# Performance work log

Hardware: AMD Instinct MI355X
Metric: run time of the kernel (lower is better)

The kernel has to match this reference:

```python
import jax, jax.numpy as jnp
import numpy as np

D_MSA = 256
D_PAIR = 128
N_HEADS = 8
HEAD_DIM = D_MSA // N_HEADS
EPS = 1e-5


def setup_inputs() -> dict:
    key = jax.random.key(0)
    ks = jax.random.split(key, 14)
    s = 0.02
    return {
        "msa": jax.random.normal(ks[0], (1, 64, 256, D_MSA), dtype=jnp.float32),
        "pair": jax.random.normal(ks[1], (1, 256, 256, D_PAIR), dtype=jnp.float32),
        "Wq": jax.random.normal(ks[2], (D_MSA, D_MSA), dtype=jnp.float32) * s,
        "bq": jnp.zeros((D_MSA,), jnp.float32),
        "Wk": jax.random.normal(ks[3], (D_MSA, D_MSA), dtype=jnp.float32) * s,
        "bk": jnp.zeros((D_MSA,), jnp.float32),
        "Wv": jax.random.normal(ks[4], (D_MSA, D_MSA), dtype=jnp.float32) * s,
        "bv": jnp.zeros((D_MSA,), jnp.float32),
        "Wpb": jax.random.normal(ks[5], (D_PAIR, N_HEADS), dtype=jnp.float32) * s,
        "bpb": jnp.zeros((N_HEADS,), jnp.float32),
        "Wo": jax.random.normal(ks[6], (D_MSA, D_MSA), dtype=jnp.float32) * s,
        "bo": jnp.zeros((D_MSA,), jnp.float32),
        "gamma": jnp.ones((D_MSA,), jnp.float32),
        "beta": jnp.zeros((D_MSA,), jnp.float32),
    }


def reference(msa, pair, Wq, bq, Wk, bk, Wv, bv, Wpb, bpb, Wo, bo, gamma, beta):
    B, N, L, D = msa.shape
    H, Hd = N_HEADS, HEAD_DIM
    # projections -> (B, N, L, H, Hd)
    q = (msa @ Wq + bq).reshape(B, N, L, H, Hd)
    k = (msa @ Wk + bk).reshape(B, N, L, H, Hd)
    v = (msa @ Wv + bv).reshape(B, N, L, H, Hd)
    # scores: (B, N, H, L, L)
    scores = jnp.einsum('bnihd,bnjhd->bnhij', q, k) / jnp.sqrt(jnp.float32(Hd))
    # pair bias: (B, L, L, H) -> (B, H, L, L), broadcast over N
    pb = jnp.transpose(pair @ Wpb + bpb, (0, 3, 1, 2))
    scores = scores + pb[:, None]
    attn = jax.nn.softmax(scores, axis=-1)
    attn_out = jnp.einsum('bnhij,bnjhd->bnihd', attn, v).reshape(B, N, L, D)
    attn_out = attn_out @ Wo + bo
    # residual + LayerNorm
    x = msa + attn_out
    mu = jnp.mean(x, axis=-1, keepdims=True)
    var = jnp.var(x, axis=-1, keepdims=True)
    return (x - mu) * jax.lax.rsqrt(var + EPS) * gamma + beta
```

## Files before the change

### kernel.cpp

```cpp
#include <hip/hip_runtime.h>

#define NSEQ 64
#define LL   256
#define DD   256
#define HH   8
#define HDIM 32

typedef short short8  __attribute__((ext_vector_type(8)));
typedef short short4v __attribute__((ext_vector_type(4)));
typedef float float4v __attribute__((ext_vector_type(4)));

#define MFMA16(a,b,c) __builtin_amdgcn_mfma_f32_16x16x32_bf16((a),(b),(c),0,0,0)

__device__ __forceinline__ float4v zero4() {
  float4v z;
  z[0] = 0.f; z[1] = 0.f; z[2] = 0.f; z[3] = 0.f;
  return z;
}

__device__ __forceinline__ short f2b(float f) {
  unsigned u = __float_as_uint(f);
  u = (u + 0x7fffu + ((u >> 16) & 1u)) >> 16;
  return (short)u;
}

__device__ __forceinline__ float b2f(short s) {
  return __uint_as_float(((unsigned)(unsigned short)s) << 16);
}

__device__ __forceinline__ short8 cvt8(const float* p) {
  float4 a = *(const float4*)p;
  float4 b = *(const float4*)(p + 4);
  short8 r;
  r[0] = f2b(a.x); r[1] = f2b(a.y); r[2] = f2b(a.z); r[3] = f2b(a.w);
  r[4] = f2b(b.x); r[5] = f2b(b.y); r[6] = f2b(b.z); r[7] = f2b(b.w);
  return r;
}

__device__ __forceinline__ void ld_lds16(const void* g, void* l) {
  __builtin_amdgcn_global_load_lds(
      (const __attribute__((address_space(1))) unsigned int*)g,
      (__attribute__((address_space(3))) unsigned int*)l, 16, 0, 0);
}
#define WAIT_VM0() __builtin_amdgcn_s_waitcnt(0x0F70)

#define WT_OFF    0
#define PB_OFF    (4*65536*2)
#define PBF_OFF   (PB_OFF + 8*65536*2)
#define Q_OFF     (PB_OFF + 8*65536*4)
#define K_OFF     (Q_OFF  + 16384*256*2)
#define VT_OFF    (K_OFF  + 16384*256*2)
#define MSA16_OFF (VT_OFF + 16384*256*2)
#define O_OFF     MSA16_OFF

__global__ __launch_bounds__(256) void k1_prep(
    const float* __restrict__ msa,  const float* __restrict__ pair,
    const float* __restrict__ Wq,   const float* __restrict__ Wk,
    const float* __restrict__ Wv,   const float* __restrict__ Wpb,
    const float* __restrict__ bpb,  const float* __restrict__ Wo,
    char* __restrict__ ws)
{
  __shared__ short ldsWt[16 * 136];
  int bx = blockIdx.x, tid = threadIdx.x;
  if (bx < 256) {
    short* pb16 = (short*)(ws + PB_OFF);
    for (int i = tid; i < 16 * 136; i += 256) ldsWt[i] = 0;
    __syncthreads();
    {
      float4 wv4 = *(const float4*)&Wpb[tid * 4];
      int kk = (tid * 4) >> 3, n0 = (tid * 4) & 7;
      ldsWt[(n0 + 0) * 136 + kk] = f2b(wv4.x);
      ldsWt[(n0 + 1) * 136 + kk] = f2b(wv4.y);
      ldsWt[(n0 + 2) * 136 + kk] = f2b(wv4.z);
      ldsWt[(n0 + 3) * 136 + kk] = f2b(wv4.w);
    }
    __syncthreads();
    int w = tid >> 6, l = tid & 63, q = l >> 4, c = l & 15;
    int base = bx * 256 + w * 64;
    float bias = bpb[c & 7];
    short8 bf[4];
#pragma unroll
    for (int ks = 0; ks < 4; ks++)
      bf[ks] = *(const short8*)&ldsWt[c * 136 + ks * 32 + q * 8];
    float4v acc[4];
#pragma unroll
    for (int mt = 0; mt < 4; mt++) acc[mt] = zero4();
#pragma unroll
    for (int ks = 0; ks < 4; ks++) {
#pragma unroll
      for (int mt = 0; mt < 4; mt++) {
        short8 af = cvt8(&pair[(base + mt * 16 + c) * 128 + ks * 32 + q * 8]);
        acc[mt] = MFMA16(af, bf[ks], acc[mt]);
      }
    }
    if (c < 8) {
#pragma unroll
      for (int mt = 0; mt < 4; mt++) {
        short4v o;
#pragma unroll
        for (int r = 0; r < 4; r++) o[r] = f2b(acc[mt][r] + bias);
        *(short4v*)&pb16[c * 65536 + base + mt * 16 + q * 4] = o;
      }
    }
  } else if (bx < 1280) {
    int b2 = bx - 256;
    int mat = b2 >> 8, r = b2 & 255;
    const float* W = (mat == 0) ? Wq : (mat == 1) ? Wk : (mat == 2) ? Wv : Wo;
    short* wt = (short*)(ws + WT_OFF) + mat * 65536;
    wt[tid * 256 + r] = f2b(W[r * 256 + tid]);
  } else {
    int b3 = bx - 1280;
    const float* src = msa + b3 * 8192;
    short* dst = (short*)(ws + MSA16_OFF) + b3 * 8192;
#pragma unroll
    for (int i = 0; i < 8; i++) {
      int idx = i * 1024 + tid * 4;
      float4 v = *(const float4*)&src[idx];
      short4v s;
      s[0] = f2b(v.x); s[1] = f2b(v.y); s[2] = f2b(v.z); s[3] = f2b(v.w);
      *(short4v*)&dst[idx] = s;
    }
  }
}

__global__ __launch_bounds__(256) void k2_qkv(
    const float* __restrict__ bq, const float* __restrict__ bk,
    const float* __restrict__ bv, char* __restrict__ ws)
{
  __shared__ __align__(16) short lsA[128 * 128];
  __shared__ __align__(16) short lsB[128 * 128];
  int bx = blockIdx.x, tid = threadIdx.x;
  if (bx >= 768) {
    int b = bx - 768;
    int it16 = b & 15;
    const short* src = (const short*)(ws + PB_OFF) + (b >> 4) * 65536 + it16 * 4096;
    short* pbf = (short*)(ws + PBF_OFF);
    short* lt = lsA;
#pragma unroll
    for (int i2 = 0; i2 < 2; i2++) {
      int idx = i2 * 2048 + tid * 8;
      *(short8*)&lt[(idx >> 8) * 264 + (idx & 255)] = *(const short8*)&src[idx];
    }
    __syncthreads();
#pragma unroll
    for (int i2 = 0; i2 < 4; i2++) {
      int fid = i2 * 256 + tid;
      int jt = fid >> 6, lane = fid & 63;
      int qp = lane >> 4, cp = lane & 15;
      short4v v;
#pragma unroll
      for (int r = 0; r < 4; r++)
        v[r] = lt[(qp * 4 + r) * 264 + jt * 16 + cp];
      *(short4v*)&pbf[((b * 16 + jt) * 64 + lane) * 4] = v;
    }
    return;
  }
  int rt = bx & 127, ct = bx >> 7;
  int m = ct >> 1, cb = (ct & 1) * 128;
  int R0 = rt * 128;
  const short* msa16 = (const short*)(ws + MSA16_OFF);
  const short* wt = (const short*)(ws + WT_OFF) + m * 65536;
  int w = tid >> 6, l = tid & 63, q = l >> 4, c = l & 15;
  int WR = (w & 1) * 64, WC = (w >> 1) * 64;
  float4v acc[4][4];
#pragma unroll
  for (int mt = 0; mt < 4; mt++)
#pragma unroll
    for (int nt = 0; nt < 4; nt++) acc[mt][nt] = zero4();

#pragma unroll 1
  for (int kk = 0; kk < 2; kk++) {
    if (kk) __syncthreads();
#pragma unroll
    for (int i = 0; i < 8; i++) {
      int ci = i * 256 + tid;
      int r = ci >> 4, pos = ci & 15;
      int kc = pos ^ (r & 7);
      ld_lds16(&msa16[(R0 + r) * 256 + kk * 128 + kc * 8], &lsA[ci * 8]);
    }
#pragma unroll
    for (int i = 0; i < 8; i++) {
      int ci = i * 256 + tid;
      int r = ci >> 4, pos = ci & 15;
      int kc = pos ^ (r & 7);
      ld_lds16(&wt[(cb + r) * 256 + kk * 128 + kc * 8], &lsB[ci * 8]);
    }
    WAIT_VM0();
    __syncthreads();
#pragma unroll
    for (int ks = 0; ks < 4; ks++) {
      short8 af[4], bf[4];
#pragma unroll
      for (int mt = 0; mt < 4; mt++) {
        int r = WR + mt * 16 + c;
        int phys = (ks * 4 + q) ^ (r & 7);
        af[mt] = *(const short8*)&lsA[r * 128 + phys * 8];
      }
#pragma unroll
      for (int nt = 0; nt < 4; nt++) {
        int r = WC + nt * 16 + c;
        int phys = (ks * 4 + q) ^ (r & 7);
        bf[nt] = *(const short8*)&lsB[r * 128 + phys * 8];
      }
#pragma unroll
      for (int mt = 0; mt < 4; mt++)
#pragma unroll
        for (int nt = 0; nt < 4; nt++)
          acc[mt][nt] = MFMA16(af[mt], bf[nt], acc[mt][nt]);
    }
  }

  const float* bp = (m == 0) ? bq : (m == 1) ? bk : bv;
  int n = R0 >> 8;
  if (m < 2) {
    short* dst = (short*)(ws + (m == 0 ? Q_OFF : K_OFF));
#pragma unroll
    for (int nt = 0; nt < 4; nt++) {
      int ch = cb + WC + nt * 16 + c;
      float bb = bp[ch];
      int h = ch >> 5, hd = ch & 31;
#pragma unroll
      for (int mt = 0; mt < 4; mt++) {
        int i0 = (R0 & 255) + WR + mt * 16 + q * 4;
#pragma unroll
        for (int r = 0; r < 4; r++)
          dst[((n * HH + h) * 256 + i0 + r) * HDIM + hd] = f2b(acc[mt][nt][r] + bb);
      }
    }
  } else {
    short* vt = (short*)(ws + VT_OFF);
#pragma unroll
    for (int nt = 0; nt < 4; nt++) {
      int ch = cb + WC + nt * 16 + c;
      float bb = bp[ch];
#pragma unroll
      for (int mt = 0; mt < 4; mt++) {
        int j0 = (R0 & 255) + WR + mt * 16 + q * 4;
        short4v s4;
#pragma unroll
        for (int r = 0; r < 4; r++) s4[r] = f2b(acc[mt][nt][r] + bb);
        *(short4v*)&vt[((n * HH + (ch >> 5)) * HDIM + (ch & 31)) * 256 + j0] = s4;
      }
    }
  }
}

__global__ __launch_bounds__(256) void k3_attn(char* __restrict__ ws)
{
  __shared__ __align__(16) short lds[25088];
  short* lsK = lds;
  short* lsP = lds;
  short* lsV = lds + 16896;
  int bx = blockIdx.x, tid = threadIdx.x;
  int qq = bx >> 9, grp = bx & 511;
  int n = grp >> 3, h = grp & 7;
  int w = tid >> 6, l = tid & 63, q = l >> 4, c = l & 15;
  const short* qh = (const short*)(ws + Q_OFF) + (n * HH + h) * 256 * HDIM;
  const short* kh = (const short*)(ws + K_OFF) + (n * HH + h) * 256 * HDIM;
  const short* vt = (const short*)(ws + VT_OFF) + (n * HH + h) * HDIM * 256;
  const short* pbf = (const short*)(ws + PBF_OFF) + (h * 16 + qq * 4 + w) * 16 * 256;
  short* os = (short*)(ws + O_OFF);
  const float scale = 0.17677669529663687f;
  int i0 = qq * 64 + w * 16;

  short8 aq = *(const short8*)&qh[(i0 + c) * HDIM + q * 8];

#pragma unroll
  for (int i = 0; i < 4; i++) {
    int ci = i * 256 + tid;
    ld_lds16(&kh[ci * 8], &lsK[ci * 8]);
  }
#pragma unroll
  for (int i = 0; i < 4; i++) {
    int ci = i * 256 + tid;
    int row = ci >> 5, j = ci & 31;
    int sj = j ^ (row & 7);
    ld_lds16(&vt[row * 256 + sj * 8], &lsV[ci * 8]);
  }
  WAIT_VM0();
  __syncthreads();

  float4v s[16];
#pragma unroll
  for (int jt = 0; jt < 16; jt++) {
    short8 bk8 = *(const short8*)&lsK[(jt * 16 + c) * 32 + q * 8];
    s[jt] = MFMA16(aq, bk8, zero4());
  }
#pragma unroll
  for (int jt = 0; jt < 16; jt++) {
    short4v pv = *(const short4v*)&pbf[(jt * 64 + l) * 4];
#pragma unroll
    for (int r = 0; r < 4; r++)
      s[jt][r] = __builtin_fmaf(s[jt][r], scale, b2f(pv[r]));
  }
  float inv[4];
#pragma unroll
  for (int r = 0; r < 4; r++) {
    float m = s[0][r];
#pragma unroll
    for (int jt = 1; jt < 16; jt++) m = fmaxf(m, s[jt][r]);
    m = fmaxf(m, __shfl_xor(m, 1, 64));
    m = fmaxf(m, __shfl_xor(m, 2, 64));
    m = fmaxf(m, __shfl_xor(m, 4, 64));
    m = fmaxf(m, __shfl_xor(m, 8, 64));
    float rs = 0.f;
#pragma unroll
    for (int jt = 0; jt < 16; jt++) {
      float p = __expf(s[jt][r] - m);
      s[jt][r] = p;
      rs += p;
    }
    rs += __shfl_xor(rs, 1, 64);
    rs += __shfl_xor(rs, 2, 64);
    rs += __shfl_xor(rs, 4, 64);
    rs += __shfl_xor(rs, 8, 64);
    inv[r] = 1.f / rs;
  }
  __syncthreads();
#pragma unroll
  for (int jt = 0; jt < 16; jt++)
#pragma unroll
    for (int r = 0; r < 4; r++)
      lsP[(w * 16 + q * 4 + r) * 264 + jt * 16 + c] = f2b(s[jt][r]);
  float4v o0 = zero4(), o1 = zero4();
#pragma unroll
  for (int kk = 0; kk < 8; kk++) {
    short8 ap = *(const short8*)&lsP[(w * 16 + c) * 264 + kk * 32 + q * 8];
    int sl0 = ((kk * 4 + q) ^ (c & 7)) * 8;
    short8 b0 = *(const short8*)&lsV[c * 256 + sl0];
    short8 b1 = *(const short8*)&lsV[(16 + c) * 256 + sl0];
    o0 = MFMA16(ap, b0, o0);
    o1 = MFMA16(ap, b1, o1);
  }
#pragma unroll
  for (int r = 0; r < 4; r++) {
    os[(n * 256 + i0 + q * 4 + r) * 256 + h * 32 + c]      = f2b(o0[r] * inv[r]);
    os[(n * 256 + i0 + q * 4 + r) * 256 + h * 32 + 16 + c] = f2b(o1[r] * inv[r]);
  }
}

__global__ __launch_bounds__(256) void k4_out(
    const float* __restrict__ msa, const float* __restrict__ bo,
    const float* __restrict__ gamma, const float* __restrict__ beta,
    const char* __restrict__ ws, float* __restrict__ out)
{
  __shared__ __align__(16) short lsA[32 * 128];
  __shared__ __align__(16) short lsB[256 * 128];
  __shared__ float sred[2][32][2];
  int bx = blockIdx.x, tid = threadIdx.x;
  int w = tid >> 6, l = tid & 63, q = l >> 4, c = l & 15;
  int rg = w >> 1, ch2 = w & 1;
  int R0 = bx * 32;
  int Rw = R0 + rg * 16;
  int C0 = ch2 * 128;
  const short* osrc = (const short*)(ws + O_OFF);
  const short* wto  = (const short*)(ws + WT_OFF) + 3 * 65536;

  float4v acc[8];
#pragma unroll
  for (int nt = 0; nt < 8; nt++) acc[nt] = zero4();

#pragma unroll 1
  for (int kk = 0; kk < 2; kk++) {
    if (kk) __syncthreads();
#pragma unroll
    for (int i = 0; i < 2; i++) {
      int ci = i * 256 + tid;
      int r = ci >> 4, pos = ci & 15;
      int kc = pos ^ (r & 7);
      ld_lds16(&osrc[(R0 + r) * 256 + kk * 128 + kc * 8], &lsA[ci * 8]);
    }
#pragma unroll
    for (int i = 0; i < 16; i++) {
      int ci = i * 256 + tid;
      int r = ci >> 4, pos = ci & 15;
      int kc = pos ^ (r & 7);
      ld_lds16(&wto[r * 256 + kk * 128 + kc * 8], &lsB[ci * 8]);
    }
    WAIT_VM0();
    __syncthreads();
#pragma unroll
    for (int ks = 0; ks < 4; ks++) {
      int rA = rg * 16 + c;
      int physA = (ks * 4 + q) ^ (rA & 7);
      short8 af = *(const short8*)&lsA[rA * 128 + physA * 8];
#pragma unroll
      for (int nt = 0; nt < 8; nt++) {
        int rB = C0 + nt * 16 + c;
        int phys = (ks * 4 + q) ^ (rB & 7);
        short8 bf = *(const short8*)&lsB[rB * 128 + phys * 8];
        acc[nt] = MFMA16(af, bf, acc[nt]);
      }
    }
  }

  float s1[4] = {0, 0, 0, 0}, s2[4] = {0, 0, 0, 0};
#pragma unroll
  for (int nt = 0; nt < 8; nt++) {
    float bb = bo[C0 + nt * 16 + c];
#pragma unroll
    for (int r = 0; r < 4; r++) {
      float x = acc[nt][r] + bb + msa[(Rw + q * 4 + r) * 256 + C0 + nt * 16 + c];
      acc[nt][r] = x;
      s1[r] += x;
      s2[r] = __builtin_fmaf(x, x, s2[r]);
    }
  }
#pragma unroll
  for (int r = 0; r < 4; r++) {
    s1[r] += __shfl_xor(s1[r], 1, 64); s2[r] += __shfl_xor(s2[r], 1, 64);
    s1[r] += __shfl_xor(s1[r], 2, 64); s2[r] += __shfl_xor(s2[r], 2, 64);
    s1[r] += __shfl_xor(s1[r], 4, 64); s2[r] += __shfl_xor(s2[r], 4, 64);
    s1[r] += __shfl_xor(s1[r], 8, 64); s2[r] += __shfl_xor(s2[r], 8, 64);
  }
  if (c == 0) {
#pragma unroll
    for (int r = 0; r < 4; r++) {
      sred[0][rg * 16 + q * 4 + r][ch2] = s1[r];
      sred[1][rg * 16 + q * 4 + r][ch2] = s2[r];
    }
  }
  __syncthreads();
  float mu[4], rsd[4];
#pragma unroll
  for (int r = 0; r < 4; r++) {
    int row = rg * 16 + q * 4 + r;
    float a = sred[0][row][0] + sred[0][row][1];
    float b = sred[1][row][0] + sred[1][row][1];
    float m = a * (1.f / 256.f);
    float v = __builtin_fmaf(-m, m, b * (1.f / 256.f));
    mu[r] = m;
    rsd[r] = rsqrtf(v + 1e-5f);
  }
#pragma unroll
  for (int nt = 0; nt < 8; nt++) {
    float g = gamma[C0 + nt * 16 + c], bt = beta[C0 + nt * 16 + c];
#pragma unroll
    for (int r = 0; r < 4; r++)
      out[(Rw + q * 4 + r) * 256 + C0 + nt * 16 + c] =
          (acc[nt][r] - mu[r]) * rsd[r] * g + bt;
  }
}

extern "C" void kernel_launch(void* const* d_in, const int* in_sizes, int n_in,
                              void* d_out, int out_size, void* d_ws, size_t ws_size,
                              hipStream_t stream)
{
  const float* msa   = (const float*)d_in[0];
  const float* pair  = (const float*)d_in[1];
  const float* Wq    = (const float*)d_in[2];
  const float* bq    = (const float*)d_in[3];
  const float* Wk    = (const float*)d_in[4];
  const float* bk    = (const float*)d_in[5];
  const float* Wv    = (const float*)d_in[6];
  const float* bv    = (const float*)d_in[7];
  const float* Wpb   = (const float*)d_in[8];
  const float* bpb   = (const float*)d_in[9];
  const float* Wo    = (const float*)d_in[10];
  const float* bo    = (const float*)d_in[11];
  const float* gamma = (const float*)d_in[12];
  const float* beta  = (const float*)d_in[13];
  char* ws = (char*)d_ws;
  float* out = (float*)d_out;

  hipLaunchKernelGGL(k1_prep, dim3(1792), dim3(256), 0, stream,
                     msa, pair, Wq, Wk, Wv, Wpb, bpb, Wo, ws);
  hipLaunchKernelGGL(k2_qkv, dim3(896), dim3(256), 0, stream,
                     bq, bk, bv, ws);
  hipLaunchKernelGGL(k3_attn, dim3(2048), dim3(256), 0, stream, ws);
  hipLaunchKernelGGL(k4_out, dim3(512), dim3(256), 0, stream,
                     msa, bo, gamma, beta, ws, out);
}
```

Measured before the change: 167.7 us.

## Coalesce pair-bias loads, weight transpose, and QKV epilogue stores via LDS staging

The pair-bias GEMM now stages each wave's pair rows into swizzled LDS with coalesced float4 loads, replacing strided per-lane global reads. The weight transpose uses 64x64 tiles transposed through LDS with vectorized writes instead of one scalar element per thread, which cuts the k1 grid. The Q/K/V epilogue in k2 writes the accumulator tile to LDS and then emits 16-byte coalesced global stores instead of scattered 2-byte stores. These changes add LDS footprint and extra barriers in exchange for better global memory coalescing.

```diff
diff --git a/kernel.cpp b/kernel.cpp
--- a/kernel.cpp
+++ b/kernel.cpp
@@ -26,15 +26,6 @@
 
 __device__ __forceinline__ float b2f(short s) {
   return __uint_as_float(((unsigned)(unsigned short)s) << 16);
-}
-
-__device__ __forceinline__ short8 cvt8(const float* p) {
-  float4 a = *(const float4*)p;
-  float4 b = *(const float4*)(p + 4);
-  short8 r;
-  r[0] = f2b(a.x); r[1] = f2b(a.y); r[2] = f2b(a.z); r[3] = f2b(a.w);
-  r[4] = f2b(b.x); r[5] = f2b(b.y); r[6] = f2b(b.z); r[7] = f2b(b.w);
-  return r;
 }
 
 __device__ __forceinline__ void ld_lds16(const void* g, void* l) {
@@ -60,6 +51,7 @@
     const float* __restrict__ bpb,  const float* __restrict__ Wo,
     char* __restrict__ ws)
 {
+  __shared__ __align__(16) short shm[4 * 64 * 128];
   __shared__ short ldsWt[16 * 136];
   int bx = blockIdx.x, tid = threadIdx.x;
   if (bx < 256) {
@@ -77,6 +69,19 @@
     __syncthreads();
     int w = tid >> 6, l = tid & 63, q = l >> 4, c = l & 15;
     int base = bx * 256 + w * 64;
+    short* lsWw = shm + w * 8192;
+#pragma unroll
+    for (int it = 0; it < 16; it++) {
+      int jl = it * 4 + (l >> 4);
+      int kc = l & 15;
+      const float* src = &pair[(base + jl) * 128 + kc * 8];
+      float4 a = *(const float4*)src;
+      float4 b = *(const float4*)(src + 4);
+      short8 v8;
+      v8[0] = f2b(a.x); v8[1] = f2b(a.y); v8[2] = f2b(a.z); v8[3] = f2b(a.w);
+      v8[4] = f2b(b.x); v8[5] = f2b(b.y); v8[6] = f2b(b.z); v8[7] = f2b(b.w);
+      *(short8*)&lsWw[jl * 128 + ((kc ^ (jl & 7)) * 8)] = v8;
+    }
     float bias = bpb[c & 7];
     short8 bf[4];
 #pragma unroll
@@ -89,7 +94,8 @@
     for (int ks = 0; ks < 4; ks++) {
 #pragma unroll
       for (int mt = 0; mt < 4; mt++) {
-        short8 af = cvt8(&pair[(base + mt * 16 + c) * 128 + ks * 32 + q * 8]);
+        int row = mt * 16 + c;
+        short8 af = *(const short8*)&lsWw[row * 128 + (((ks * 4 + q) ^ (c & 7)) * 8)];
         acc[mt] = MFMA16(af, bf[ks], acc[mt]);
       }
     }
@@ -102,14 +108,33 @@
         *(short4v*)&pb16[c * 65536 + base + mt * 16 + q * 4] = o;
       }
     }
-  } else if (bx < 1280) {
+  } else if (bx < 320) {
     int b2 = bx - 256;
-    int mat = b2 >> 8, r = b2 & 255;
+    int mat = b2 >> 4, sub = b2 & 15;
+    int k0 = (sub >> 2) * 64, n0 = (sub & 3) * 64;
     const float* W = (mat == 0) ? Wq : (mat == 1) ? Wk : (mat == 2) ? Wv : Wo;
     short* wt = (short*)(ws + WT_OFF) + mat * 65536;
-    wt[tid * 256 + r] = f2b(W[r * 256 + tid]);
+    short* ldsT = shm;
+#pragma unroll
+    for (int p = 0; p < 4; p++) {
+      int kl = p * 16 + (tid >> 4);
+      int nl = (tid & 15) * 4;
+      float4 v = *(const float4*)&W[(k0 + kl) * 256 + n0 + nl];
+      ldsT[(nl + 0) * 72 + kl] = f2b(v.x);
+      ldsT[(nl + 1) * 72 + kl] = f2b(v.y);
+      ldsT[(nl + 2) * 72 + kl] = f2b(v.z);
+      ldsT[(nl + 3) * 72 + kl] = f2b(v.w);
+    }
+    __syncthreads();
+#pragma unroll
+    for (int p = 0; p < 2; p++) {
+      int id = p * 256 + tid;
+      int nl = id >> 3, c8 = id & 7;
+      *(short8*)&wt[(n0 + nl) * 256 + k0 + c8 * 8] =
+          *(const short8*)&ldsT[nl * 72 + c8 * 8];
+    }
   } else {
-    int b3 = bx - 1280;
+    int b3 = bx - 320;
     const float* src = msa + b3 * 8192;
     short* dst = (short*)(ws + MSA16_OFF) + b3 * 8192;
 #pragma unroll
@@ -127,8 +152,9 @@
     const float* __restrict__ bq, const float* __restrict__ bk,
     const float* __restrict__ bv, char* __restrict__ ws)
 {
-  __shared__ __align__(16) short lsA[128 * 128];
-  __shared__ __align__(16) short lsB[128 * 128];
+  __shared__ __align__(16) short ls[2 * 128 * 128];
+  short* lsA = ls;
+  short* lsB = ls + 16384;
   int bx = blockIdx.x, tid = threadIdx.x;
   if (bx >= 768) {
     int b = bx - 768;
@@ -212,35 +238,52 @@
 
   const float* bp = (m == 0) ? bq : (m == 1) ? bk : bv;
   int n = R0 >> 8;
+  __syncthreads();
+  short* lsC = ls;
   if (m < 2) {
-    short* dst = (short*)(ws + (m == 0 ? Q_OFF : K_OFF));
 #pragma unroll
     for (int nt = 0; nt < 4; nt++) {
-      int ch = cb + WC + nt * 16 + c;
-      float bb = bp[ch];
-      int h = ch >> 5, hd = ch & 31;
-#pragma unroll
-      for (int mt = 0; mt < 4; mt++) {
-        int i0 = (R0 & 255) + WR + mt * 16 + q * 4;
+      float bb = bp[cb + WC + nt * 16 + c];
+#pragma unroll
+      for (int mt = 0; mt < 4; mt++)
 #pragma unroll
         for (int r = 0; r < 4; r++)
-          dst[((n * HH + h) * 256 + i0 + r) * HDIM + hd] = f2b(acc[mt][nt][r] + bb);
-      }
+          lsC[(WR + mt * 16 + q * 4 + r) * 136 + WC + nt * 16 + c] =
+              f2b(acc[mt][nt][r] + bb);
+    }
+    __syncthreads();
+    short* dst = (short*)(ws + (m == 0 ? Q_OFF : K_OFF)) + n * 65536;
+    int ibase = R0 & 255;
+#pragma unroll
+    for (int p = 0; p < 8; p++) {
+      int id = p * 256 + tid;
+      int il = id >> 4, ch8 = id & 15;
+      int chg = cb + ch8 * 8;
+      int hh = chg >> 5, hd0 = chg & 31;
+      *(short8*)&dst[(hh * 256 + ibase + il) * 32 + hd0] =
+          *(const short8*)&lsC[il * 136 + ch8 * 8];
     }
   } else {
-    short* vt = (short*)(ws + VT_OFF);
 #pragma unroll
     for (int nt = 0; nt < 4; nt++) {
-      int ch = cb + WC + nt * 16 + c;
-      float bb = bp[ch];
-#pragma unroll
-      for (int mt = 0; mt < 4; mt++) {
-        int j0 = (R0 & 255) + WR + mt * 16 + q * 4;
-        short4v s4;
-#pragma unroll
-        for (int r = 0; r < 4; r++) s4[r] = f2b(acc[mt][nt][r] + bb);
-        *(short4v*)&vt[((n * HH + (ch >> 5)) * HDIM + (ch & 31)) * 256 + j0] = s4;
-      }
+      float bb = bp[cb + WC + nt * 16 + c];
+#pragma unroll
+      for (int mt = 0; mt < 4; mt++)
+#pragma unroll
+        for (int r = 0; r < 4; r++)
+          lsC[(WC + nt * 16 + c) * 136 + WR + mt * 16 + q * 4 + r] =
+              f2b(acc[mt][nt][r] + bb);
+    }
+    __syncthreads();
+    short* vt = (short*)(ws + VT_OFF) + n * 65536;
+    int jbase = R0 & 255;
+#pragma unroll
+    for (int p = 0; p < 8; p++) {
+      int id = p * 256 + tid;
+      int chl = id >> 4, j8 = id & 15;
+      int chg = cb + chl;
+      *(short8*)&vt[chg * 256 + jbase + j8 * 8] =
+          *(const short8*)&lsC[chl * 136 + j8 * 8];
     }
   }
 }
@@ -463,7 +506,7 @@
   char* ws = (char*)d_ws;
   float* out = (float*)d_out;
 
-  hipLaunchKernelGGL(k1_prep, dim3(1792), dim3(256), 0, stream,
+  hipLaunchKernelGGL(k1_prep, dim3(832), dim3(256), 0, stream,
                      msa, pair, Wq, Wk, Wv, Wpb, bpb, Wo, ws);
   hipLaunchKernelGGL(k2_qkv, dim3(896), dim3(256), 0, stream,
                      bq, bk, bv, ws);
```

Result: faster. 158.0 us (-5.8%).
